# Optimization experiments

Hardware: AMD Instinct MI355X
Metric: run time of the kernel (lower is better)

## Reference

```python
import jax, jax.numpy as jnp
import numpy as np

B, D = 1048576, 64  # batch, series length


def _expit_m1(t):
    # R -> (-1, 1)
    return 2.0 * jax.nn.sigmoid(t) - 1.0


def _precision_ar1(param, dim):
    # Tridiagonal AR(1) precision: I + coef * (superdiag + subdiag)
    p = _expit_m1(param)                      # shape (1,)
    coef = -p / (1.0 + p ** 2)                # shape (1,)
    off = jnp.eye(dim, k=1) + jnp.eye(dim, k=-1)
    return jnp.eye(dim) + coef * off          # (dim, dim)


def setup_inputs() -> dict:
    key = jax.random.key(0)
    k1, k2, k3 = jax.random.split(key, 3)
    y_true = jax.random.normal(k1, (B, D), dtype=jnp.float32)
    y_pred = jax.random.normal(k2, (B, D), dtype=jnp.float32)
    # per-row valid lengths in [1, D] (avoid 0 to keep out/n finite)
    n = jax.random.randint(k3, (B,), 1, D + 1)
    param = jnp.zeros((1,), dtype=jnp.float32)  # nn.Parameter(torch.zeros(1))
    return {"y_true": y_true, "y_pred": y_pred, "param": param, "n": n}


def reference(y_true, y_pred, param, n):
    dim = y_true.shape[-1]
    # filter_by_n: zero out positions t >= n[b]
    mask = (jnp.arange(dim)[None, :] < n[:, None]).astype(y_true.dtype)
    diff = (y_true - y_pred) * mask           # (B, D)
    P = _precision_ar1(param, dim)            # (D, D)
    # diag(diff @ P @ diff.T) computed as batched quadratic form, O(B*D^2)
    quad = jnp.einsum('bi,ij,bj->b', diff, P, diff)  # (B,)
    return jnp.mean(quad / n.astype(y_true.dtype))
```

## Files before the change

kernel.cpp:

```cpp
#include <hip/hip_runtime.h>

#define BLOCK 256
#define UNROLL 8

__global__ __launch_bounds__(BLOCK) void mahal_kernel(
    const float4* __restrict__ yt4,
    const float4* __restrict__ yp4,
    const float*  __restrict__ param,
    const int*    __restrict__ n,
    float* __restrict__ out,
    int total_vec4,
    float invB)
{
    float t = param[0];
    float p = 2.0f / (1.0f + __expf(-t)) - 1.0f;
    float coef2 = -2.0f * p / (1.0f + p * p);

    const int chunk = BLOCK * UNROLL;
    int base = blockIdx.x * chunk + (int)threadIdx.x;

    float4 a[UNROLL], b[UNROLL];
    int veff[UNROLL];

    #pragma unroll
    for (int j = 0; j < UNROLL; ++j) {
        int gj = base + j * BLOCK;
        int g  = gj < total_vec4 ? gj : total_vec4 - 1;
        a[j] = yt4[g];
        b[j] = yp4[g];
        veff[j] = (gj < total_vec4) ? n[g >> 4] : 0;
    }

    int col4 = threadIdx.x & 15;
    int e0   = col4 << 2;
    bool not_last = (col4 != 15);
    float acc = 0.0f;

    #pragma unroll
    for (int j = 0; j < UNROLL; ++j) {
        int v = veff[j];
        float d0 = (e0 + 0 < v) ? (a[j].x - b[j].x) : 0.0f;
        float d1 = (e0 + 1 < v) ? (a[j].y - b[j].y) : 0.0f;
        float d2 = (e0 + 2 < v) ? (a[j].z - b[j].z) : 0.0f;
        float d3 = (e0 + 3 < v) ? (a[j].w - b[j].w) : 0.0f;
        float nb = __shfl_down(d0, 1, 64);
        float sumsq = d0 * d0 + d1 * d1 + d2 * d2 + d3 * d3;
        float cross = d0 * d1 + d1 * d2 + d2 * d3;
        if (not_last) cross += d3 * nb;
        float q = fmaf(coef2, cross, sumsq);
        acc = fmaf(q, __builtin_amdgcn_rcpf((float)v), acc);
    }

    #pragma unroll
    for (int off = 32; off >= 1; off >>= 1)
        acc += __shfl_down(acc, off, 64);

    __shared__ float smem[BLOCK / 64];
    int lane = threadIdx.x & 63;
    int wid  = threadIdx.x >> 6;
    if (lane == 0) smem[wid] = acc;
    __syncthreads();
    if (threadIdx.x == 0) {
        float s = 0.0f;
        #pragma unroll
        for (int i = 0; i < BLOCK / 64; ++i) s += smem[i];
        atomicAdd(out, s * invB);
    }
}

extern "C" void kernel_launch(void* const* d_in, const int* in_sizes, int n_in,
                              void* d_out, int out_size, void* d_ws, size_t ws_size,
                              hipStream_t stream) {
    const float* y_true = (const float*)d_in[0];
    const float* y_pred = (const float*)d_in[1];
    const float* param  = (const float*)d_in[2];
    const int*   n      = (const int*)d_in[3];
    float* out = (float*)d_out;

    int total = in_sizes[0];
    int B     = in_sizes[3];
    int total_vec4 = total / 4;
    float invB = 1.0f / (float)B;

    hipMemsetAsync(out, 0, sizeof(float) * out_size, stream);

    const int chunk = BLOCK * UNROLL;
    int blocks = (total_vec4 + chunk - 1) / chunk;
    mahal_kernel<<<blocks, BLOCK, 0, stream>>>((const float4*)y_true,
                                               (const float4*)y_pred,
                                               param, n, out,
                                               total_vec4, invB);
}
```

Before: 520.2 us.

## Replace global atomic accumulation with per-block partials and a finish kernel

Each block now writes its partial sum to workspace instead of doing an atomicAdd on one output float, and a second single-block kernel reduces the partials and applies the 1/B scale. This removes the memset and the contention on one address across thousands of blocks. The loads also get a fast path with no bounds checks for full blocks, plus a scheduling barrier after them. In exchange there is an extra kernel launch, and the result now depends on the workspace being at least as large as the block count.

Measured after the change: 505.1 us. 1.03x faster.

```diff
diff --git a/kernel.cpp b/kernel.cpp
--- a/kernel.cpp
+++ b/kernel.cpp
@@ -2,34 +2,44 @@
 
 #define BLOCK 256
 #define UNROLL 8
+#define CHUNK (BLOCK * UNROLL)
 
-__global__ __launch_bounds__(BLOCK) void mahal_kernel(
+__global__ __launch_bounds__(BLOCK) void mahal_main(
     const float4* __restrict__ yt4,
     const float4* __restrict__ yp4,
     const float*  __restrict__ param,
     const int*    __restrict__ n,
-    float* __restrict__ out,
-    int total_vec4,
-    float invB)
+    float* __restrict__ partial,
+    int total_vec4)
 {
     float t = param[0];
     float p = 2.0f / (1.0f + __expf(-t)) - 1.0f;
     float coef2 = -2.0f * p / (1.0f + p * p);
 
-    const int chunk = BLOCK * UNROLL;
-    int base = blockIdx.x * chunk + (int)threadIdx.x;
+    int base = blockIdx.x * CHUNK + (int)threadIdx.x;
 
     float4 a[UNROLL], b[UNROLL];
-    int veff[UNROLL];
+    int    vv[UNROLL];
 
-    #pragma unroll
-    for (int j = 0; j < UNROLL; ++j) {
-        int gj = base + j * BLOCK;
-        int g  = gj < total_vec4 ? gj : total_vec4 - 1;
-        a[j] = yt4[g];
-        b[j] = yp4[g];
-        veff[j] = (gj < total_vec4) ? n[g >> 4] : 0;
+    if ((blockIdx.x + 1) * CHUNK <= total_vec4) {
+        #pragma unroll
+        for (int j = 0; j < UNROLL; ++j) {
+            int g = base + j * BLOCK;
+            a[j]  = yt4[g];
+            b[j]  = yp4[g];
+            vv[j] = n[g >> 4];
+        }
+    } else {
+        #pragma unroll
+        for (int j = 0; j < UNROLL; ++j) {
+            int gj = base + j * BLOCK;
+            int g  = gj < total_vec4 ? gj : 0;
+            a[j]  = yt4[g];
+            b[j]  = yp4[g];
+            vv[j] = (gj < total_vec4) ? n[g >> 4] : 0;
+        }
     }
+    __builtin_amdgcn_sched_barrier(0);
 
     int col4 = threadIdx.x & 15;
     int e0   = col4 << 2;
@@ -38,7 +48,7 @@
 
     #pragma unroll
     for (int j = 0; j < UNROLL; ++j) {
-        int v = veff[j];
+        int v = vv[j];
         float d0 = (e0 + 0 < v) ? (a[j].x - b[j].x) : 0.0f;
         float d1 = (e0 + 1 < v) ? (a[j].y - b[j].y) : 0.0f;
         float d2 = (e0 + 2 < v) ? (a[j].z - b[j].z) : 0.0f;
@@ -47,8 +57,9 @@
         float sumsq = d0 * d0 + d1 * d1 + d2 * d2 + d3 * d3;
         float cross = d0 * d1 + d1 * d2 + d2 * d3;
         if (not_last) cross += d3 * nb;
-        float q = fmaf(coef2, cross, sumsq);
-        acc = fmaf(q, __builtin_amdgcn_rcpf((float)v), acc);
+        float q  = fmaf(coef2, cross, sumsq);
+        float rv = __builtin_amdgcn_rcpf((float)(v > 0 ? v : 1));
+        acc = fmaf(q, rv, acc);
     }
 
     #pragma unroll
@@ -64,8 +75,37 @@
         float s = 0.0f;
         #pragma unroll
         for (int i = 0; i < BLOCK / 64; ++i) s += smem[i];
-        atomicAdd(out, s * invB);
+        partial[blockIdx.x] = s;
     }
+}
+
+__global__ __launch_bounds__(256) void mahal_finish(
+    const float* __restrict__ partial,
+    float* __restrict__ out,
+    int nblocks, float invB)
+{
+    float acc = 0.0f;
+    if ((nblocks & 3) == 0) {
+        const float4* p4 = (const float4*)partial;
+        int n4 = nblocks >> 2;
+        for (int i = threadIdx.x; i < n4; i += 256) {
+            float4 v = p4[i];
+            acc += v.x + v.y + v.z + v.w;
+        }
+    } else {
+        for (int i = threadIdx.x; i < nblocks; i += 256)
+            acc += partial[i];
+    }
+    #pragma unroll
+    for (int off = 32; off >= 1; off >>= 1)
+        acc += __shfl_down(acc, off, 64);
+    __shared__ float smem[4];
+    int lane = threadIdx.x & 63;
+    int wid  = threadIdx.x >> 6;
+    if (lane == 0) smem[wid] = acc;
+    __syncthreads();
+    if (threadIdx.x == 0)
+        out[0] = (smem[0] + smem[1] + smem[2] + smem[3]) * invB;
 }
 
 extern "C" void kernel_launch(void* const* d_in, const int* in_sizes, int n_in,
@@ -82,12 +122,11 @@
     int total_vec4 = total / 4;
     float invB = 1.0f / (float)B;
 
-    hipMemsetAsync(out, 0, sizeof(float) * out_size, stream);
+    int blocks = (total_vec4 + CHUNK - 1) / CHUNK;
+    float* partial = (float*)d_ws;
 
-    const int chunk = BLOCK * UNROLL;
-    int blocks = (total_vec4 + chunk - 1) / chunk;
-    mahal_kernel<<<blocks, BLOCK, 0, stream>>>((const float4*)y_true,
-                                               (const float4*)y_pred,
-                                               param, n, out,
-                                               total_vec4, invB);
+    mahal_main<<<blocks, BLOCK, 0, stream>>>((const float4*)y_true,
+                                             (const float4*)y_pred,
+                                             param, n, partial, total_vec4);
+    mahal_finish<<<1, 256, 0, stream>>>(partial, out, blocks, invB);
 }
```
